# Kernel tuning notes

Measured on AMD Instinct MI355X. Metric: run time of the kernel, lower is better.

## Reference

```python
import jax, jax.numpy as jnp
import numpy as np

N = 40000      # nodes
E = 640000     # edges (avg degree 16)
D = 128        # feature dim (in_features == all hidden_dims due to residual)


def setup_inputs() -> dict:
    key = jax.random.key(0)
    ks = jax.random.split(key, 8)
    xavier = (6.0 / (D + D)) ** 0.5
    return {
        "x": jax.random.normal(ks[0], (N, D), dtype=jnp.float32),
        "edge_index": jax.random.randint(ks[1], (2, E), 0, N, dtype=jnp.int64),
        "W_t": jax.random.uniform(ks[2], (D, D), jnp.float32, -xavier, xavier),
        "b_t": jnp.zeros((D,), jnp.float32),
        "W0": jax.random.uniform(ks[3], (D, D), jnp.float32, -xavier, xavier),
        "b0": jnp.zeros((D,), jnp.float32),
        "W1": jax.random.uniform(ks[4], (D, D), jnp.float32, -xavier, xavier),
        "b1": jnp.zeros((D,), jnp.float32),
    }


def _gcn_layer(h, row, col, W, b):
    # linear transform, then edge-wise gather + scatter-add aggregation
    z = jnp.matmul(h, W)                                  # [N, D]
    agg = jnp.zeros_like(z).at[row].add(z[col])           # out[row] += z[col]
    return jax.nn.relu(agg + b)


def reference(x, edge_index, W_t, b_t, W0, b0, W1, b1):
    row, col = edge_index[0], edge_index[1]
    h = jnp.matmul(x, W_t) + b_t                          # self.transform
    # residual GCN layers (dropout p=0.0 -> identity; eval mode)
    h = h + _gcn_layer(h, row, col, W0, b0)
    h = h + _gcn_layer(h, row, col, W1, b1)
    return h
```

## Files before the change

### kernel.cpp

```cpp
#include <hip/hip_runtime.h>
#include <hip/hip_bf16.h>

#define N_NODES 40000
#define N_EDGES 640000
#define DIM     128
#define NB      157
#define GEMMB   625
#define HEB     1250
#define CHUNKS  64
#define CHUNK_E 10000
#define LDSW    10000

#define HIST0   65

typedef __attribute__((ext_vector_type(8))) short short8;
typedef __attribute__((ext_vector_type(4))) float f32x4;
typedef __attribute__((ext_vector_type(2))) float f32x2;

__device__ inline short f2bf(float f) {
    __hip_bfloat16 h = __float2bfloat16(f);
    return *reinterpret_cast<short*>(&h);
}
__device__ inline float bf2f(short u) {
    union { unsigned int i; float f; } x;
    x.i = ((unsigned int)(unsigned short)u) << 16;
    return x.f;
}

__device__ inline int fragidx(int k, int n) {
    int kb = k >> 5, kq = (k >> 3) & 3, j = k & 7;
    int nt = n >> 4, nl = n & 15;
    return (((kb * 8 + nt) * 64 + kq * 16 + nl) * 8 + j);
}

__global__ __launch_bounds__(256) void prep_hist_zero(const float* __restrict__ Wt,
                                                      const float* __restrict__ W0,
                                                      const float* __restrict__ W1,
                                                      const float* __restrict__ bt,
                                                      short* __restrict__ WtF,
                                                      short* __restrict__ WfF,
                                                      short* __restrict__ W1F,
                                                      float* __restrict__ btf,
                                                      int* __restrict__ flagtot,
                                                      const int* __restrict__ rows,
                                                      unsigned char* __restrict__ rank8,
                                                      unsigned int* __restrict__ cnt8w) {
    __shared__ unsigned int lcnt[LDSW];
    const int b = blockIdx.x;

    if (b < 64) {
        int gid = b * 256 + threadIdx.x;
        int k = gid >> 7, n = gid & 127;
        float wf = 0.f;
        for (int kk = 0; kk < 128; ++kk)
            wf += Wt[k * 128 + kk] * W0[kk * 128 + n];
        int fi = fragidx(k, n);
        WtF[fi] = f2bf(Wt[k * 128 + n]);
        W1F[fi] = f2bf(W1[k * 128 + n]);
        WfF[fi] = f2bf(wf);
        if (gid < 128) {
            float s = 0.f;
            for (int kk = 0; kk < 128; ++kk) s += bt[kk] * W0[kk * 128 + n];
            btf[n] = s;
        }
    } else if (b == 64) {
        flagtot[threadIdx.x]       = 0;
        flagtot[threadIdx.x + 256] = 0;
    } else {
        for (int i = threadIdx.x; i < LDSW; i += 256) lcnt[i] = 0u;
        __syncthreads();
        const int base = (b - HIST0) * CHUNK_E;
#pragma unroll
        for (int i = 0; i < 40; ++i) {
            int o = i * 256 + threadIdx.x;
            if (o < CHUNK_E) {
                int e = base + o;
                int r = rows[e];
                unsigned int sh = (unsigned int)(r & 3) * 8u;
                unsigned int old = atomicAdd(&lcnt[r >> 2], 1u << sh);
                rank8[e] = (unsigned char)((old >> sh) & 0xFFu);
            }
        }
        __syncthreads();
        unsigned int* out = cnt8w + (size_t)(b - HIST0) * LDSW;
        for (int i = threadIdx.x; i < LDSW; i += 256) out[i] = lcnt[i];
    }
}

__global__ __launch_bounds__(256) void scan_onepass(unsigned char* __restrict__ cnt8,
                                                    int* __restrict__ flags,
                                                    int* __restrict__ totals,
                                                    int* __restrict__ row_ptr) {
    __shared__ int sh[256];
    const int b = blockIdx.x;
    const int t = threadIdx.x;
    const int i = b * 256 + t;

    int deg = 0;
    if (i < N_NODES) {
#pragma unroll 8
        for (int c = 0; c < CHUNKS; ++c) deg += cnt8[(size_t)c * N_NODES + i];
    }

    int val = deg;
    sh[t] = val;
    __syncthreads();
    for (int off = 1; off < 256; off <<= 1) {
        int a = (t >= off) ? sh[t - off] : 0;
        __syncthreads();
        val += a;
        sh[t] = val;
        __syncthreads();
    }
    const int excl  = val - deg;
    const int total = sh[255];

    if (t == 0) {
        atomicExch(&totals[b], total);
        __threadfence();
        atomicExch(&flags[b], 1);
    }

    int v = 0;
    if (t < NB) {
        while (atomicAdd(&flags[t], 0) == 0) { }
        v = atomicAdd(&totals[t], 0);
    }
    __syncthreads();
    int val2 = v;
    sh[t] = val2;
    __syncthreads();
    for (int off = 1; off < 256; off <<= 1) {
        int a = (t >= off) ? sh[t - off] : 0;
        __syncthreads();
        val2 += a;
        sh[t] = val2;
        __syncthreads();
    }
    int blkOff = (b == 0) ? 0 : sh[b - 1];

    if (i < N_NODES) {
        int base = excl + blkOff;
        row_ptr[i] = base;
        int run = 0;
#pragma unroll 8
        for (int c = 0; c < CHUNKS; ++c) {
            int cv = cnt8[(size_t)c * N_NODES + i];
            cnt8[(size_t)c * N_NODES + i] = (unsigned char)run;
            run += cv;
        }
    }
    if (i == 0) row_ptr[N_NODES] = N_EDGES;
}

__global__ __launch_bounds__(256) void gemm_scatter(const float* __restrict__ A,
                                                    const short* __restrict__ WtF,
                                                    const short* __restrict__ WfF,
                                                    const float* __restrict__ bt,
                                                    const float* __restrict__ btf,
                                                    float* __restrict__ H,
                                                    __hip_bfloat16* __restrict__ Z,
                                                    const int* __restrict__ rows,
                                                    const int* __restrict__ cols,
                                                    const unsigned char* __restrict__ rank8,
                                                    const unsigned char* __restrict__ pref8,
                                                    const int* __restrict__ row_ptr,
                                                    unsigned short* __restrict__ adj) {
    const int blk = blockIdx.x;
    const int t   = threadIdx.x;

    if (blk < GEMMB) {
        const int wave = t >> 6;
        const int l    = t & 63;
        const int nl   = l & 15;
        const int quad = l >> 4;
        const int wRow = blk * 64 + wave * 16;

        f32x4 accH[8], accZ[8];
#pragma unroll
        for (int nt = 0; nt < 8; ++nt) {
            accH[nt] = (f32x4){0.f, 0.f, 0.f, 0.f};
            accZ[nt] = (f32x4){0.f, 0.f, 0.f, 0.f};
        }

#pragma unroll
        for (int kb = 0; kb < 4; ++kb) {
            const float* ap = A + (size_t)(wRow + nl) * 128 + kb * 32 + quad * 8;
            float4 f0 = *(const float4*)ap;
            float4 f1 = *(const float4*)(ap + 4);
            short8 afrag;
            afrag[0] = f2bf(f0.x); afrag[1] = f2bf(f0.y);
            afrag[2] = f2bf(f0.z); afrag[3] = f2bf(f0.w);
            afrag[4] = f2bf(f1.x); afrag[5] = f2bf(f1.y);
            afrag[6] = f2bf(f1.z); afrag[7] = f2bf(f1.w);
#pragma unroll
            for (int nt = 0; nt < 8; ++nt) {
                int off = ((kb * 8 + nt) * 64 + l) * 8;
                short8 bt_frag = *(const short8*)&WtF[off];
                short8 bf_frag = *(const short8*)&WfF[off];
                accH[nt] = __builtin_amdgcn_mfma_f32_16x16x32_bf16(afrag, bt_frag, accH[nt], 0, 0, 0);
                accZ[nt] = __builtin_amdgcn_mfma_f32_16x16x32_bf16(afrag, bf_frag, accZ[nt], 0, 0, 0);
            }
        }

#pragma unroll
        for (int nt = 0; nt < 8; ++nt) {
            int col = nt * 16 + nl;
            float bH = bt[col];
            float bZ = btf[col];
#pragma unroll
            for (int r = 0; r < 4; ++r) {
                int row = wRow + quad * 4 + r;
                H[(size_t)row * 128 + col] = accH[nt][r] + bH;
                *(short*)&Z[(size_t)row * 128 + col] = f2bf(accZ[nt][r] + bZ);
            }
        }
        return;
    }

    int gid = (blk - GEMMB) * 256 + t;
#pragma unroll
    for (int h = 0; h < 2; ++h) {
        int e = gid + h * HEB * 256;
        int r = rows[e];
        int c = e / CHUNK_E;
        int pos = row_ptr[r] + (int)pref8[(size_t)c * N_NODES + r] + (int)rank8[e];
        adj[pos] = (unsigned short)cols[e];
    }
}

__global__ __launch_bounds__(256) void agg0_gemm(const __hip_bfloat16* __restrict__ z0,
                                                 const int* __restrict__ row_ptr,
                                                 const unsigned short* __restrict__ adj,
                                                 const float* __restrict__ bias,
                                                 const short* __restrict__ W1F,
                                                 float* __restrict__ H,
                                                 unsigned char* __restrict__ Z1) {
    __shared__ short hs[16][136];

    const int t    = threadIdx.x;
    const int wave = t >> 6;
    const int l    = t & 63;
    const int quad = l >> 4;
    const int sl   = l & 15;
    const int nodeBase = blockIdx.x * 16;
    const int m    = wave * 4 + quad;
    const int node = nodeBase + m;

    const int s = row_ptr[node];
    const int e = row_ptr[node + 1];

    float acc[8];
#pragma unroll
    for (int j = 0; j < 8; ++j) acc[j] = 0.f;

    const __hip_bfloat16* zb = z0 + sl * 8;
    int it = s;
    for (; it + 7 < e; it += 8) {
        int c0 = adj[it + 0], c1 = adj[it + 1], c2 = adj[it + 2], c3 = adj[it + 3];
        int c4 = adj[it + 4], c5 = adj[it + 5], c6 = adj[it + 6], c7 = adj[it + 7];
        short8 v0 = *(const short8*)&zb[(size_t)c0 * DIM];
        short8 v1 = *(const short8*)&zb[(size_t)c1 * DIM];
        short8 v2 = *(const short8*)&zb[(size_t)c2 * DIM];
        short8 v3 = *(const short8*)&zb[(size_t)c3 * DIM];
        short8 v4 = *(const short8*)&zb[(size_t)c4 * DIM];
        short8 v5 = *(const short8*)&zb[(size_t)c5 * DIM];
        short8 v6 = *(const short8*)&zb[(size_t)c6 * DIM];
        short8 v7 = *(const short8*)&zb[(size_t)c7 * DIM];
#pragma unroll
        for (int j = 0; j < 8; ++j)
            acc[j] += ((bf2f(v0[j]) + bf2f(v1[j])) + (bf2f(v2[j]) + bf2f(v3[j]))) +
                      ((bf2f(v4[j]) + bf2f(v5[j])) + (bf2f(v6[j]) + bf2f(v7[j])));
    }
    for (; it + 3 < e; it += 4) {
        int c0 = adj[it + 0], c1 = adj[it + 1], c2 = adj[it + 2], c3 = adj[it + 3];
        short8 v0 = *(const short8*)&zb[(size_t)c0 * DIM];
        short8 v1 = *(const short8*)&zb[(size_t)c1 * DIM];
        short8 v2 = *(const short8*)&zb[(size_t)c2 * DIM];
        short8 v3 = *(const short8*)&zb[(size_t)c3 * DIM];
#pragma unroll
        for (int j = 0; j < 8; ++j)
            acc[j] += (bf2f(v0[j]) + bf2f(v1[j])) + (bf2f(v2[j]) + bf2f(v3[j]));
    }
    for (; it + 1 < e; it += 2) {
        int c0 = adj[it + 0], c1 = adj[it + 1];
        short8 v0 = *(const short8*)&zb[(size_t)c0 * DIM];
        short8 v1 = *(const short8*)&zb[(size_t)c1 * DIM];
#pragma unroll
        for (int j = 0; j < 8; ++j) acc[j] += bf2f(v0[j]) + bf2f(v1[j]);
    }
    if (it < e) {
        int c = adj[it];
        short8 v = *(const short8*)&zb[(size_t)c * DIM];
#pragma unroll
        for (int j = 0; j < 8; ++j) acc[j] += bf2f(v[j]);
    }

    {
        float* hp = H + (size_t)node * DIM + sl * 8;
        float4 h0 = *(float4*)hp;
        float4 h1 = *(float4*)(hp + 4);
        float4 b0v = *(const float4*)&bias[sl * 8];
        float4 b1v = *(const float4*)&bias[sl * 8 + 4];
        float r[8];
        r[0] = acc[0] + b0v.x; r[1] = acc[1] + b0v.y; r[2] = acc[2] + b0v.z; r[3] = acc[3] + b0v.w;
        r[4] = acc[4] + b1v.x; r[5] = acc[5] + b1v.y; r[6] = acc[6] + b1v.z; r[7] = acc[7] + b1v.w;
        float hn[8];
        hn[0] = h0.x; hn[1] = h0.y; hn[2] = h0.z; hn[3] = h0.w;
        hn[4] = h1.x; hn[5] = h1.y; hn[6] = h1.z; hn[7] = h1.w;
        short8 o;
#pragma unroll
        for (int j = 0; j < 8; ++j) {
            float rr = r[j] > 0.f ? r[j] : 0.f;
            hn[j] += rr;
            o[j] = f2bf(hn[j]);
        }
        *(float4*)hp       = make_float4(hn[0], hn[1], hn[2], hn[3]);
        *(float4*)(hp + 4) = make_float4(hn[4], hn[5], hn[6], hn[7]);
        *(short8*)&hs[m][sl * 8] = o;
    }
    __syncthreads();

    f32x4 acc2[2];
    acc2[0] = (f32x4){0.f, 0.f, 0.f, 0.f};
    acc2[1] = (f32x4){0.f, 0.f, 0.f, 0.f};
#pragma unroll
    for (int kb = 0; kb < 4; ++kb) {
        short8 afrag = *(const short8*)&hs[sl][kb * 32 + quad * 8];
#pragma unroll
        for (int nt2 = 0; nt2 < 2; ++nt2) {
            int nt = wave * 2 + nt2;
            short8 bfrag = *(const short8*)&W1F[((kb * 8 + nt) * 64 + l) * 8];
            acc2[nt2] = __builtin_amdgcn_mfma_f32_16x16x32_bf16(afrag, bfrag, acc2[nt2], 0, 0, 0);
        }
    }
#pragma unroll
    for (int nt2 = 0; nt2 < 2; ++nt2) {
        int col = (wave * 2 + nt2) * 16 + sl;
#pragma unroll
        for (int r = 0; r < 4; ++r) {
            int row = nodeBase + quad * 4 + r;
            float v = acc2[nt2][r];
            int packed = __builtin_amdgcn_cvt_pk_fp8_f32(v, v, 0, false);
            Z1[(size_t)row * 128 + col] = (unsigned char)(packed & 0xFF);
        }
    }
}

__global__ __launch_bounds__(256) void agg_final(const unsigned char* __restrict__ z1,
                                                 const int* __restrict__ row_ptr,
                                                 const unsigned short* __restrict__ adj,
                                                 const float* __restrict__ bias,
                                                 float* __restrict__ H) {
    const int t    = threadIdx.x;
    const int wave = t >> 6;
    const int l    = t & 63;
    const int quad = l >> 4;
    const int sl   = l & 15;
    const int node = blockIdx.x * 16 + wave * 4 + quad;
    if (node >= N_NODES) return;

    const int s = row_ptr[node];
    const int e = row_ptr[node + 1];

    float acc[8];
#pragma unroll
    for (int j = 0; j < 8; ++j) acc[j] = 0.f;

#define ADD_FP8(u2)                                                          \
    {                                                                        \
        f32x2 a0 = __builtin_amdgcn_cvt_pk_f32_fp8((u2).x, false);           \
        f32x2 a1 = __builtin_amdgcn_cvt_pk_f32_fp8((u2).x, true);            \
        f32x2 a2 = __builtin_amdgcn_cvt_pk_f32_fp8((u2).y, false);           \
        f32x2 a3 = __builtin_amdgcn_cvt_pk_f32_fp8((u2).y, true);            \
        acc[0] += a0.x; acc[1] += a0.y; acc[2] += a1.x; acc[3] += a1.y;      \
        acc[4] += a2.x; acc[5] += a2.y; acc[6] += a3.x; acc[7] += a3.y;      \
    }

    const unsigned char* zb = z1 + sl * 8;
    int it = s;
    for (; it + 7 < e; it += 8) {
        int c0 = adj[it + 0], c1 = adj[it + 1], c2 = adj[it + 2], c3 = adj[it + 3];
        int c4 = adj[it + 4], c5 = adj[it + 5], c6 = adj[it + 6], c7 = adj[it + 7];
        uint2 v0 = *(const uint2*)&zb[(size_t)c0 * 128];
        uint2 v1 = *(const uint2*)&zb[(size_t)c1 * 128];
        uint2 v2 = *(const uint2*)&zb[(size_t)c2 * 128];
        uint2 v3 = *(const uint2*)&zb[(size_t)c3 * 128];
        uint2 v4 = *(const uint2*)&zb[(size_t)c4 * 128];
        uint2 v5 = *(const uint2*)&zb[(size_t)c5 * 128];
        uint2 v6 = *(const uint2*)&zb[(size_t)c6 * 128];
        uint2 v7 = *(const uint2*)&zb[(size_t)c7 * 128];
        ADD_FP8(v0); ADD_FP8(v1); ADD_FP8(v2); ADD_FP8(v3);
        ADD_FP8(v4); ADD_FP8(v5); ADD_FP8(v6); ADD_FP8(v7);
    }
    for (; it + 3 < e; it += 4) {
        int c0 = adj[it + 0], c1 = adj[it + 1], c2 = adj[it + 2], c3 = adj[it + 3];
        uint2 v0 = *(const uint2*)&zb[(size_t)c0 * 128];
        uint2 v1 = *(const uint2*)&zb[(size_t)c1 * 128];
        uint2 v2 = *(const uint2*)&zb[(size_t)c2 * 128];
        uint2 v3 = *(const uint2*)&zb[(size_t)c3 * 128];
        ADD_FP8(v0); ADD_FP8(v1); ADD_FP8(v2); ADD_FP8(v3);
    }
    for (; it + 1 < e; it += 2) {
        int c0 = adj[it + 0], c1 = adj[it + 1];
        uint2 v0 = *(const uint2*)&zb[(size_t)c0 * 128];
        uint2 v1 = *(const uint2*)&zb[(size_t)c1 * 128];
        ADD_FP8(v0); ADD_FP8(v1);
    }
    if (it < e) {
        int c = adj[it];
        uint2 v = *(const uint2*)&zb[(size_t)c * 128];
        ADD_FP8(v);
    }
#undef ADD_FP8

    float* hp = H + (size_t)node * DIM + sl * 8;
    float4 h0 = *(float4*)hp;
    float4 h1 = *(float4*)(hp + 4);
    float4 b0 = *(const float4*)&bias[sl * 8];
    float4 b1 = *(const float4*)&bias[sl * 8 + 4];
    float r0 = acc[0] + b0.x, r1 = acc[1] + b0.y, r2 = acc[2] + b0.z, r3 = acc[3] + b0.w;
    float r4 = acc[4] + b1.x, r5 = acc[5] + b1.y, r6 = acc[6] + b1.z, r7 = acc[7] + b1.w;
    h0.x += r0 > 0.f ? r0 : 0.f;  h0.y += r1 > 0.f ? r1 : 0.f;
    h0.z += r2 > 0.f ? r2 : 0.f;  h0.w += r3 > 0.f ? r3 : 0.f;
    h1.x += r4 > 0.f ? r4 : 0.f;  h1.y += r5 > 0.f ? r5 : 0.f;
    h1.z += r6 > 0.f ? r6 : 0.f;  h1.w += r7 > 0.f ? r7 : 0.f;
    *(float4*)hp       = h0;
    *(float4*)(hp + 4) = h1;
}

extern "C" void kernel_launch(void* const* d_in, const int* in_sizes, int n_in,
                              void* d_out, int out_size, void* d_ws, size_t ws_size,
                              hipStream_t stream) {
    const float* x   = (const float*)d_in[0];
    const int*   ei  = (const int*)d_in[1];
    const float* W_t = (const float*)d_in[2];
    const float* b_t = (const float*)d_in[3];
    const float* W0  = (const float*)d_in[4];
    const float* b0  = (const float*)d_in[5];
    const float* W1  = (const float*)d_in[6];
    const float* b1  = (const float*)d_in[7];

    const int* rows = ei;
    const int* cols = ei + N_EDGES;

    float* H = (float*)d_out;

    char* w = (char*)d_ws;
    __hip_bfloat16* Z0 = (__hip_bfloat16*)w;  w += (size_t)N_NODES * DIM * 2;
    unsigned char*  Z1 = (unsigned char*)w;   w += (size_t)N_NODES * DIM;
    short* WtF = (short*)w;  w += 128 * 128 * 2;
    short* WfF = (short*)w;  w += 128 * 128 * 2;
    short* W1F = (short*)w;  w += 128 * 128 * 2;
    float* btf = (float*)w;  w += 128 * 4;
    int* row_ptr = (int*)w;  w += (N_NODES + 1) * 4;
    int* flagtot = (int*)w;  w += 768 * 4;
    unsigned int* cnt8w = (unsigned int*)w;  w += (size_t)CHUNKS * LDSW * 4;
    unsigned char* rank8 = (unsigned char*)w;  w += (size_t)N_EDGES;
    unsigned short* adj  = (unsigned short*)w;

    int* flags  = flagtot;
    int* totals = flagtot + 256;

    prep_hist_zero<<<HIST0 + CHUNKS, 256, 0, stream>>>(W_t, W0, W1, b_t,
                                                       WtF, WfF, W1F, btf, flagtot,
                                                       rows, rank8, cnt8w);

    scan_onepass<<<NB, 256, 0, stream>>>((unsigned char*)cnt8w, flags, totals, row_ptr);

    gemm_scatter<<<GEMMB + HEB, 256, 0, stream>>>(x, WtF, WfF, b_t, btf, H, Z0,
                                                  rows, cols, rank8,
                                                  (unsigned char*)cnt8w, row_ptr, adj);

    agg0_gemm<<<N_NODES / 16, 256, 0, stream>>>(Z0, row_ptr, adj, b0, W1F, H, Z1);

    agg_final<<<(N_NODES + 15) / 16, 256, 0, stream>>>(Z1, row_ptr, adj, b1, H);
}
```

Before: 174.6 us.

## Sort nodes by degree into a permutation to balance aggregation waves

Computes a per-block degree histogram in the scan kernel, then builds a counting-sort permutation of nodes by in-degree (capped at 63) inside the fused gemm/scatter launch. Both aggregation kernels now process nodes through this permutation, so the quads of a wave handle nodes with similar degree and less time is lost to divergent loop lengths. In exchange, the extra histogram atomics and a serial prefix over earlier blocks' bins add work, and the row writes to Z1 and H become scattered, which can hurt coalescing and locality.

```diff
diff --git a/kernel.cpp b/kernel.cpp
--- a/kernel.cpp
+++ b/kernel.cpp
@@ -66,6 +66,7 @@
     } else if (b == 64) {
         flagtot[threadIdx.x]       = 0;
         flagtot[threadIdx.x + 256] = 0;
+        flagtot[threadIdx.x + 512] = 0;
     } else {
         for (int i = threadIdx.x; i < LDSW; i += 256) lcnt[i] = 0u;
         __syncthreads();
@@ -90,8 +91,12 @@
 __global__ __launch_bounds__(256) void scan_onepass(unsigned char* __restrict__ cnt8,
                                                     int* __restrict__ flags,
                                                     int* __restrict__ totals,
-                                                    int* __restrict__ row_ptr) {
+                                                    int* __restrict__ degTot,
+                                                    int* __restrict__ row_ptr,
+                                                    unsigned char* __restrict__ rankD,
+                                                    int* __restrict__ blkBin) {
     __shared__ int sh[256];
+    __shared__ int hist[64];
     const int b = blockIdx.x;
     const int t = threadIdx.x;
     const int i = b * 256 + t;
@@ -100,6 +105,18 @@
     if (i < N_NODES) {
 #pragma unroll 8
         for (int c = 0; c < CHUNKS; ++c) deg += cnt8[(size_t)c * N_NODES + i];
+    }
+
+    if (t < 64) hist[t] = 0;
+    __syncthreads();
+    int bin = deg < 63 ? deg : 63;
+    int rk = 0;
+    if (i < N_NODES) rk = atomicAdd(&hist[bin], 1);
+    __syncthreads();
+    if (i < N_NODES) rankD[i] = (unsigned char)rk;
+    if (t < 64) {
+        blkBin[b * 64 + t] = hist[t];
+        atomicAdd(&degTot[t], hist[t]);
     }
 
     int val = deg;
@@ -153,28 +170,63 @@
     if (i == 0) row_ptr[N_NODES] = N_EDGES;
 }
 
-__global__ __launch_bounds__(256) void gemm_scatter(const float* __restrict__ A,
-                                                    const short* __restrict__ WtF,
-                                                    const short* __restrict__ WfF,
-                                                    const float* __restrict__ bt,
-                                                    const float* __restrict__ btf,
-                                                    float* __restrict__ H,
-                                                    __hip_bfloat16* __restrict__ Z,
-                                                    const int* __restrict__ rows,
-                                                    const int* __restrict__ cols,
-                                                    const unsigned char* __restrict__ rank8,
-                                                    const unsigned char* __restrict__ pref8,
-                                                    const int* __restrict__ row_ptr,
-                                                    unsigned short* __restrict__ adj) {
+__global__ __launch_bounds__(256) void perm_gemm_scatter(const float* __restrict__ A,
+                                                         const short* __restrict__ WtF,
+                                                         const short* __restrict__ WfF,
+                                                         const float* __restrict__ bt,
+                                                         const float* __restrict__ btf,
+                                                         float* __restrict__ H,
+                                                         __hip_bfloat16* __restrict__ Z,
+                                                         const int* __restrict__ rows,
+                                                         const int* __restrict__ cols,
+                                                         const unsigned char* __restrict__ rank8,
+                                                         const unsigned char* __restrict__ pref8,
+                                                         const int* __restrict__ row_ptr,
+                                                         unsigned short* __restrict__ adj,
+                                                         const unsigned char* __restrict__ rankD,
+                                                         const int* __restrict__ blkBin,
+                                                         const int* __restrict__ degTot,
+                                                         int* __restrict__ perm) {
+    __shared__ int blockPre[64];
+    __shared__ int binStart[64];
     const int blk = blockIdx.x;
     const int t   = threadIdx.x;
 
-    if (blk < GEMMB) {
+    if (blk < NB) {
+        if (t < 64) {
+            int acc = 0;
+            for (int b2 = 0; b2 < blk; ++b2) acc += blkBin[b2 * 64 + t];
+            blockPre[t] = acc;
+        } else if (t >= 64 && t < 128) {
+            binStart[t - 64] = degTot[t - 64];
+        }
+        __syncthreads();
+        if (t == 0) {
+            int run = 0;
+#pragma unroll
+            for (int d = 0; d < 64; ++d) {
+                int c = binStart[d];
+                binStart[d] = run;
+                run += c;
+            }
+        }
+        __syncthreads();
+        int i = blk * 256 + t;
+        if (i < N_NODES) {
+            int deg = row_ptr[i + 1] - row_ptr[i];
+            int bin = deg < 63 ? deg : 63;
+            int slot = binStart[bin] + blockPre[bin] + (int)rankD[i];
+            perm[slot] = i;
+        }
+        return;
+    }
+
+    if (blk < NB + GEMMB) {
         const int wave = t >> 6;
         const int l    = t & 63;
         const int nl   = l & 15;
         const int quad = l >> 4;
-        const int wRow = blk * 64 + wave * 16;
+        const int wRow = (blk - NB) * 64 + wave * 16;
 
         f32x4 accH[8], accZ[8];
 #pragma unroll
@@ -218,7 +270,7 @@
         return;
     }
 
-    int gid = (blk - GEMMB) * 256 + t;
+    int gid = (blk - NB - GEMMB) * 256 + t;
 #pragma unroll
     for (int h = 0; h < 2; ++h) {
         int e = gid + h * HEB * 256;
@@ -234,18 +286,22 @@
                                                  const unsigned short* __restrict__ adj,
                                                  const float* __restrict__ bias,
                                                  const short* __restrict__ W1F,
+                                                 const int* __restrict__ perm,
                                                  float* __restrict__ H,
                                                  unsigned char* __restrict__ Z1) {
     __shared__ short hs[16][136];
+    __shared__ int sperm[16];
 
     const int t    = threadIdx.x;
     const int wave = t >> 6;
     const int l    = t & 63;
     const int quad = l >> 4;
     const int sl   = l & 15;
-    const int nodeBase = blockIdx.x * 16;
     const int m    = wave * 4 + quad;
-    const int node = nodeBase + m;
+
+    if (t < 16) sperm[t] = perm[blockIdx.x * 16 + t];
+    __syncthreads();
+    const int node = sperm[m];
 
     const int s = row_ptr[node];
     const int e = row_ptr[node + 1];
@@ -339,10 +395,10 @@
         int col = (wave * 2 + nt2) * 16 + sl;
 #pragma unroll
         for (int r = 0; r < 4; ++r) {
-            int row = nodeBase + quad * 4 + r;
+            int rowNode = sperm[quad * 4 + r];
             float v = acc2[nt2][r];
             int packed = __builtin_amdgcn_cvt_pk_fp8_f32(v, v, 0, false);
-            Z1[(size_t)row * 128 + col] = (unsigned char)(packed & 0xFF);
+            Z1[(size_t)rowNode * 128 + col] = (unsigned char)(packed & 0xFF);
         }
     }
 }
@@ -351,14 +407,14 @@
                                                  const int* __restrict__ row_ptr,
                                                  const unsigned short* __restrict__ adj,
                                                  const float* __restrict__ bias,
+                                                 const int* __restrict__ perm,
                                                  float* __restrict__ H) {
     const int t    = threadIdx.x;
     const int wave = t >> 6;
     const int l    = t & 63;
     const int quad = l >> 4;
     const int sl   = l & 15;
-    const int node = blockIdx.x * 16 + wave * 4 + quad;
-    if (node >= N_NODES) return;
+    const int node = perm[blockIdx.x * 16 + wave * 4 + quad];
 
     const int s = row_ptr[node];
     const int e = row_ptr[node + 1];
@@ -457,22 +513,28 @@
     int* flagtot = (int*)w;  w += 768 * 4;
     unsigned int* cnt8w = (unsigned int*)w;  w += (size_t)CHUNKS * LDSW * 4;
     unsigned char* rank8 = (unsigned char*)w;  w += (size_t)N_EDGES;
-    unsigned short* adj  = (unsigned short*)w;
+    unsigned short* adj  = (unsigned short*)w;  w += (size_t)N_EDGES * 2;
+    unsigned char* rankD = (unsigned char*)w;  w += (size_t)N_NODES;
+    int* blkBin = (int*)w;  w += (size_t)NB * 64 * 4;
+    int* perm   = (int*)w;  w += (size_t)N_NODES * 4;
 
     int* flags  = flagtot;
     int* totals = flagtot + 256;
+    int* degTot = flagtot + 512;
 
     prep_hist_zero<<<HIST0 + CHUNKS, 256, 0, stream>>>(W_t, W0, W1, b_t,
                                                        WtF, WfF, W1F, btf, flagtot,
                                                        rows, rank8, cnt8w);
 
-    scan_onepass<<<NB, 256, 0, stream>>>((unsigned char*)cnt8w, flags, totals, row_ptr);
-
-    gemm_scatter<<<GEMMB + HEB, 256, 0, stream>>>(x, WtF, WfF, b_t, btf, H, Z0,
-                                                  rows, cols, rank8,
-                                                  (unsigned char*)cnt8w, row_ptr, adj);
-
-    agg0_gemm<<<N_NODES / 16, 256, 0, stream>>>(Z0, row_ptr, adj, b0, W1F, H, Z1);
-
-    agg_final<<<(N_NODES + 15) / 16, 256, 0, stream>>>(Z1, row_ptr, adj, b1, H);
-}
+    scan_onepass<<<NB, 256, 0, stream>>>((unsigned char*)cnt8w, flags, totals,
+                                         degTot, row_ptr, rankD, blkBin);
+
+    perm_gemm_scatter<<<NB + GEMMB + HEB, 256, 0, stream>>>(x, WtF, WfF, b_t, btf, H, Z0,
+                                                            rows, cols, rank8,
+                                                            (unsigned char*)cnt8w, row_ptr, adj,
+                                                            rankD, blkBin, degTot, perm);
+
+    agg0_gemm<<<N_NODES / 16, 256, 0, stream>>>(Z0, row_ptr, adj, b0, W1F, perm, H, Z1);
+
+    agg_final<<<N_NODES / 16, 256, 0, stream>>>(Z1, row_ptr, adj, b1, perm, H);
+}
```

Measured after the change: 188.1 us. 1.08x slower.
